# Kernel tuning notes

Hardware: AMD Instinct MI355X
Metric: run time of the kernel (lower is better)

Reference implementation:

```python
import jax, jax.numpy as jnp
import numpy as np

D_MODEL = 1024
N_HIDDEN = 64   # per-head dim (outer factor of packed proj dim)
N_HEAD = 16
B, L = 2, 2048


def setup_inputs() -> dict:
    key = jax.random.key(0)
    ks = jax.random.split(key, 7)
    s = 0.02
    return {
        "q": jax.random.normal(ks[0], (B, L, D_MODEL), dtype=jnp.float32),
        "k": jax.random.normal(ks[1], (B, L, D_MODEL), dtype=jnp.float32),
        "v": jax.random.normal(ks[2], (B, L, D_MODEL), dtype=jnp.float32),
        # torch nn.Linear weights: shape (out_features, in_features), y = x @ W.T
        "W_Q": jax.random.normal(ks[3], (N_HIDDEN * N_HEAD, D_MODEL), dtype=jnp.float32) * s,
        "W_K": jax.random.normal(ks[4], (N_HIDDEN * N_HEAD, D_MODEL), dtype=jnp.float32) * s,
        "W_V": jax.random.normal(ks[5], (N_HIDDEN * N_HEAD, D_MODEL), dtype=jnp.float32) * s,
        "W_O": jax.random.normal(ks[6], (D_MODEL, N_HEAD * N_HIDDEN), dtype=jnp.float32) * s,
    }


def reference(q, k, v, W_Q, W_K, W_V, W_O):
    b, l, _ = q.shape
    # projections (bias=False)
    qp = q @ W_Q.T  # [b,l,n_hidden*n_head]
    kp = k @ W_K.T
    vp = v @ W_V.T
    # rearrange 'b l (c h) -> b l c h' with c=n_hidden: hidden is OUTER factor
    qh = qp.reshape(b, l, N_HIDDEN, N_HEAD)
    kh = kp.reshape(b, l, N_HIDDEN, N_HEAD)
    vh = vp.reshape(b, l, N_HIDDEN, N_HEAD)
    scores = jnp.einsum('bldh,bjdh->bhlj', qh, kh) / np.float32(np.sqrt(N_HIDDEN))
    attn = jax.nn.softmax(scores, axis=-1)
    out = jnp.einsum('bhlj,bjdh->bldh', attn, vh)  # [b,l,n_hidden,n_head]
    out = out.reshape(b, l, N_HIDDEN * N_HEAD)      # 'b l d h -> b l (d h)'
    return out @ W_O.T
```

## Files before the change

### kernel.cpp

```cpp
#include <hip/hip_runtime.h>
#include <hip/hip_bf16.h>
#include <stdint.h>

typedef __attribute__((ext_vector_type(8))) short short8;
typedef __attribute__((ext_vector_type(4))) float f32x4;
typedef __attribute__((ext_vector_type(16))) float f32x16;
typedef __attribute__((ext_vector_type(2))) int int2v;
typedef unsigned short u16;
typedef unsigned int u32;


#define WAIT_VM8() do { asm volatile("s_waitcnt vmcnt(8)" ::: "memory"); \
                        __builtin_amdgcn_sched_barrier(0); } while (0)
#define WAIT_VM0() do { asm volatile("s_waitcnt vmcnt(0)" ::: "memory"); \
                        __builtin_amdgcn_sched_barrier(0); } while (0)
#define BARRIER()  do { __builtin_amdgcn_s_barrier(); \
                        __builtin_amdgcn_sched_barrier(0); } while (0)

__device__ __forceinline__ u16 bf16rne(float f) {
  u32 u = __builtin_bit_cast(u32, f);
  u += 0x7FFFu + ((u >> 16) & 1u);
  return (u16)(u >> 16);
}

__device__ __forceinline__ u32 cvtpk(float lo, float hi) {
  u32 r;
  asm("v_cvt_pk_bf16_f32 %0, %1, %2" : "=v"(r) : "v"(lo), "v"(hi));
  return r;
}

__device__ __forceinline__ void gl_lds16(const u16* g, u16* l) {
  __builtin_amdgcn_global_load_lds((const __attribute__((address_space(1))) void*)g,
                                   (__attribute__((address_space(3))) void*)l, 16, 0, 0);
}

struct CastArgs {
  const float* src[7];
  u16* dst[7];
  int n4[7];
};

__global__ void cast_all(CastArgs a) {
  const int id = blockIdx.y;
  const float* __restrict__ s = a.src[id];
  u16* __restrict__ d = a.dst[id];
  const int stride = gridDim.x * blockDim.x;
  const int i0 = blockIdx.x * blockDim.x + threadIdx.x;
  if (id < 6) {
    const int n4 = a.n4[id];
    for (int i = i0; i < n4; i += stride) {
      float4 v = ((const float4*)s)[i];
      u32 lo = (u32)bf16rne(v.x) | ((u32)bf16rne(v.y) << 16);
      u32 hi = (u32)bf16rne(v.z) | ((u32)bf16rne(v.w) << 16);
      ((uint2*)d)[i] = make_uint2(lo, hi);
    }
  } else {
    const int n = a.n4[6];
    for (int i = i0; i < n; i += stride) {
      int row = i >> 10, c = i & 1023;
      int hh = c >> 6, dd = c & 63;
      d[i] = bf16rne(s[(row << 10) + dd * 16 + hh]);
    }
  }
}

template<int AHEADS>
__device__ __forceinline__ void gemm_body(const u16* __restrict__ A, const u16* __restrict__ Bw,
                                          void* __restrict__ Cd, int epi, float ascale) {
  const int bn = blockIdx.x * 128, bm = blockIdx.y * 128;
  const int tid = threadIdx.x, lane = tid & 63, w = tid >> 6;
  const int wr = w >> 1, wc = w & 1;
  __shared__ __align__(16) u16 As[2][128 * 64];
  __shared__ __align__(16) u16 Bs[2][128 * 64];
  f32x4 acc[4][4];
#pragma unroll
  for (int m = 0; m < 4; ++m)
#pragma unroll
    for (int n = 0; n < 4; ++n) acc[m][n] = (f32x4){0.f, 0.f, 0.f, 0.f};

  auto STAGE = [&](int kt, int b) {
#pragma unroll
    for (int i = 0; i < 4; ++i) {
      int c = tid + i * 256;
      int row = c >> 3, kc = c & 7;
      int swz = (kc ^ (row & 7)) << 3;
      const u16* srcA;
      if (AHEADS) {
        int bA = bm >> 11;
        int lrow = (bm & 2047) + row;
        srcA = A + ((size_t)(bA * 16 + kt) * 2048 + lrow) * 64 + swz;
      } else {
        srcA = A + (size_t)(bm + row) * 1024 + kt * 64 + swz;
      }
      gl_lds16(srcA, &As[b][c * 8]);
      const u16* srcB = Bw + (size_t)(bn + row) * 1024 + kt * 64 + swz;
      gl_lds16(srcB, &Bs[b][c * 8]);
    }
  };

  auto COMPUTE = [&](int b) {
#pragma unroll
    for (int ks = 0; ks < 2; ++ks) {
      const int ck = ks * 4 + (lane >> 4);
      short8 af[4], bfr[4];
#pragma unroll
      for (int m = 0; m < 4; ++m) {
        int r = wr * 64 + m * 16 + (lane & 15);
        af[m] = *(const short8*)&As[b][(r * 8 + (ck ^ (r & 7))) * 8];
      }
#pragma unroll
      for (int n = 0; n < 4; ++n) {
        int r = wc * 64 + n * 16 + (lane & 15);
        bfr[n] = *(const short8*)&Bs[b][(r * 8 + (ck ^ (r & 7))) * 8];
      }
#pragma unroll
      for (int m = 0; m < 4; ++m)
#pragma unroll
        for (int n = 0; n < 4; ++n)
          acc[m][n] = __builtin_amdgcn_mfma_f32_16x16x32_bf16(af[m], bfr[n], acc[m][n], 0, 0, 0);
    }
  };

  STAGE(0, 0);
  STAGE(1, 1);
  for (int kt = 0; kt < 15; ++kt) {
    WAIT_VM8();
    BARRIER();
    COMPUTE(kt & 1);
    BARRIER();
    if (kt < 14) STAGE(kt + 2, kt & 1);
  }
  WAIT_VM0();
  BARRIER();
  COMPUTE(1);

  const int lrow4 = (lane >> 4) << 2;
  const int h = lane & 15;
  if (epi == 0) {
    u16* D = (u16*)Cd;
    const int dbase = (bn + wc * 64) >> 4;
#pragma unroll
    for (int m = 0; m < 4; ++m)
#pragma unroll
      for (int i = 0; i < 4; ++i) {
        int R = bm + wr * 64 + m * 16 + lrow4 + i;
        int b = R >> 11, l = R & 2047;
        u32 lo = (u32)bf16rne(acc[m][0][i] * ascale) | ((u32)bf16rne(acc[m][1][i] * ascale) << 16);
        u32 hi = (u32)bf16rne(acc[m][2][i] * ascale) | ((u32)bf16rne(acc[m][3][i] * ascale) << 16);
        size_t addr = ((size_t)((b * 16 + h) * 2048 + l)) * 64 + dbase;
        *(uint2*)(D + addr) = make_uint2(lo, hi);
      }
  } else if (epi == 1) {
    u16* D = (u16*)Cd;
    const int dbase = (bn + wc * 64) >> 4;
    const int b = bm >> 11;
#pragma unroll
    for (int m = 0; m < 4; ++m) {
      int l0 = (bm & 2047) + wr * 64 + m * 16 + lrow4;
#pragma unroll
      for (int n = 0; n < 4; ++n) {
        int d = dbase + n;
        u32 lo = (u32)bf16rne(acc[m][n][0]) | ((u32)bf16rne(acc[m][n][1]) << 16);
        u32 hi = (u32)bf16rne(acc[m][n][2]) | ((u32)bf16rne(acc[m][n][3]) << 16);
        size_t addr = ((size_t)((b * 16 + h) * 64 + d)) * 2048 + l0;
        *(uint2*)(D + addr) = make_uint2(lo, hi);
      }
    }
  } else {
    float* D = (float*)Cd;
#pragma unroll
    for (int m = 0; m < 4; ++m)
#pragma unroll
      for (int i = 0; i < 4; ++i) {
        int R = bm + wr * 64 + m * 16 + lrow4 + i;
        size_t base = (size_t)R * 1024 + bn + wc * 64 + (lane & 15);
#pragma unroll
        for (int n = 0; n < 4; ++n) D[base + n * 16] = acc[m][n][i];
      }
  }
}

struct ProjArgs { const u16* A[3]; const u16* W[3]; u16* D[3]; float scale[3]; };

__global__ __launch_bounds__(256, 2) void gemm_proj(ProjArgs pa) {
  const int z = blockIdx.z;
  gemm_body<0>(pa.A[z], pa.W[z], pa.D[z], z == 2 ? 1 : 0, pa.scale[z]);
}

__global__ __launch_bounds__(256, 2) void gemm_oproj(const u16* __restrict__ A,
                                                     const u16* __restrict__ W,
                                                     float* __restrict__ C) {
  gemm_body<1>(A, W, C, 2, 1.0f);
}

__global__ __launch_bounds__(128, 2) void attn_kernel(const u16* __restrict__ Qh,
                                                      const u16* __restrict__ Kh,
                                                      const u16* __restrict__ Vt,
                                                      u16* __restrict__ Oh) {
  const int hb = blockIdx.x;
  const int qt = blockIdx.y;
  const int tid = threadIdx.x, lane = tid & 63, w = tid >> 6;
  const int l31 = lane & 31, hi = lane >> 5;
  __shared__ __align__(16) u16 Ks[2][64 * 64];
  __shared__ __align__(16) u16 Vs[3][64 * 64];

  const u16* Qg = Qh + (size_t)hb * (2048 * 64);
  const u16* Kg = Kh + (size_t)hb * (2048 * 64);
  const u16* Vg = Vt + (size_t)hb * (64 * 2048);
  const int qrow = qt * 64 + w * 32 + l31;

  short8 qf[4];
#pragma unroll
  for (int ks = 0; ks < 4; ++ks)
    qf[ks] = *(const short8*)(Qg + (size_t)qrow * 64 + ks * 16 + hi * 8);

  int rs[4], sw[4];
#pragma unroll
  for (int i = 0; i < 4; ++i) {
    int c = tid + i * 128;
    rs[i] = c >> 3;
    sw[i] = (((c & 7) ^ (rs[i] & 7)) << 3);
  }

  auto STAGE_K = [&](int t, int slot) {
    const size_t ko = (size_t)t * (64 * 64);
#pragma unroll
    for (int i = 0; i < 4; ++i) {
      int c = tid + i * 128;
      gl_lds16(Kg + ko + (size_t)rs[i] * 64 + sw[i], &Ks[slot][c * 8]);
    }
  };
  auto STAGE_V = [&](int t, int slot) {
    const int vo = t * 64;
#pragma unroll
    for (int i = 0; i < 4; ++i) {
      int c = tid + i * 128;
      gl_lds16(Vg + (size_t)rs[i] * 2048 + vo + sw[i], &Vs[slot][c * 8]);
    }
  };

  f32x16 oacc0, oacc1, SA0, SA1, SB0, SB1;
#pragma unroll
  for (int i = 0; i < 16; ++i) { oacc0[i] = 0.f; oacc1[i] = 0.f; }
  u32 pkA[16], pkB[16];
  float lrow = 0.f;

  auto QKT = [&](int kslot, f32x16& s0, f32x16& s1) {
#pragma unroll
    for (int i = 0; i < 16; ++i) { s0[i] = 0.f; s1[i] = 0.f; }
    __builtin_amdgcn_s_setprio(1);
#pragma unroll
    for (int ks = 0; ks < 4; ++ks) {
      const int ck = 2 * ks + hi;
      const int r0 = l31, r1 = 32 + l31;
      short8 k0 = *(const short8*)&Ks[kslot][(r0 * 8 + (ck ^ (r0 & 7))) * 8];
      short8 k1 = *(const short8*)&Ks[kslot][(r1 * 8 + (ck ^ (r1 & 7))) * 8];
      s0 = __builtin_amdgcn_mfma_f32_32x32x16_bf16(k0, qf[ks], s0, 0, 0, 0);
      s1 = __builtin_amdgcn_mfma_f32_32x32x16_bf16(k1, qf[ks], s1, 0, 0, 0);
    }
    __builtin_amdgcn_s_setprio(0);
  };

  auto PV = [&](const u32* pk, int vslot) {
    __builtin_amdgcn_s_setprio(1);
#pragma unroll
    for (int c = 0; c < 4; ++c) {
      union { u32 wu[4]; short8 v; } un;
      un.wu[0] = pk[c * 4 + 0]; un.wu[1] = pk[c * 4 + 1];
      un.wu[2] = pk[c * 4 + 2]; un.wu[3] = pk[c * 4 + 3];
      const int ckv = 2 * c + hi;
      const int rv0 = l31, rv1 = 32 + l31;
      short8 v0 = *(const short8*)&Vs[vslot][(rv0 * 8 + (ckv ^ (rv0 & 7))) * 8];
      short8 v1 = *(const short8*)&Vs[vslot][(rv1 * 8 + (ckv ^ (rv1 & 7))) * 8];
      oacc0 = __builtin_amdgcn_mfma_f32_32x32x16_bf16(v0, un.v, oacc0, 0, 0, 0);
      oacc1 = __builtin_amdgcn_mfma_f32_32x32x16_bf16(v1, un.v, oacc1, 0, 0, 0);
    }
    __builtin_amdgcn_s_setprio(0);
  };

  auto SOFTMAX = [&](f32x16& s0, f32x16& s1, u32* pk) {
#pragma unroll
    for (int i = 0; i < 16; ++i) {
      s0[i] = __builtin_amdgcn_exp2f(s0[i]);
      s1[i] = __builtin_amdgcn_exp2f(s1[i]);
    }
    f32x16 a01 = s0 + s1;
    float r8[8];
#pragma unroll
    for (int i = 0; i < 8; ++i) r8[i] = a01[i] + a01[i + 8];
#pragma unroll
    for (int i = 0; i < 4; ++i) r8[i] += r8[i + 4];
    float rsum = (r8[0] + r8[1]) + (r8[2] + r8[3]);
    int2v pr = __builtin_amdgcn_permlane32_swap(__builtin_bit_cast(int, rsum),
                                                __builtin_bit_cast(int, rsum), false, false);
    lrow += __builtin_bit_cast(float, pr[0]) + __builtin_bit_cast(float, pr[1]);
#pragma unroll
    for (int c = 0; c < 4; ++c) {
      float pe0, pe1, pe2, pe3, pe4, pe5, pe6, pe7;
      if (c < 2) {
        const int s8 = (c & 1) * 8;
        pe0 = s0[s8 + 0]; pe1 = s0[s8 + 1]; pe2 = s0[s8 + 2]; pe3 = s0[s8 + 3];
        pe4 = s0[s8 + 4]; pe5 = s0[s8 + 5]; pe6 = s0[s8 + 6]; pe7 = s0[s8 + 7];
      } else {
        const int s8 = (c & 1) * 8;
        pe0 = s1[s8 + 0]; pe1 = s1[s8 + 1]; pe2 = s1[s8 + 2]; pe3 = s1[s8 + 3];
        pe4 = s1[s8 + 4]; pe5 = s1[s8 + 5]; pe6 = s1[s8 + 6]; pe7 = s1[s8 + 7];
      }
      u32 a0 = cvtpk(pe0, pe1), a1 = cvtpk(pe2, pe3);
      u32 a2 = cvtpk(pe4, pe5), a3 = cvtpk(pe6, pe7);
      int2v w02 = __builtin_amdgcn_permlane32_swap((int)a0, (int)a2, false, false);
      int2v w13 = __builtin_amdgcn_permlane32_swap((int)a1, (int)a3, false, false);
      pk[c * 4 + 0] = (u32)w02[0]; pk[c * 4 + 1] = (u32)w13[0];
      pk[c * 4 + 2] = (u32)w02[1]; pk[c * 4 + 3] = (u32)w13[1];
    }
  };

  STAGE_K(0, 0); STAGE_K(1, 1); STAGE_V(0, 0);
  WAIT_VM8(); BARRIER();
  QKT(0, SA0, SA1);
  BARRIER();
  STAGE_K(2, 0); STAGE_V(1, 1);
  WAIT_VM8(); BARRIER();
  QKT(1, SB0, SB1);
  SOFTMAX(SA0, SA1, pkB);
  BARRIER();
  STAGE_K(3, 1); STAGE_V(2, 2);

  for (int i = 2; i < 32; i += 2) {
    WAIT_VM8(); BARRIER();
    QKT(0, SA0, SA1);
    PV(pkB, (i - 2) % 3);
    SOFTMAX(SB0, SB1, pkA);
    BARRIER();
    if (i + 2 <= 31) STAGE_K(i + 2, 0);
    STAGE_V(i + 1, (i + 1) % 3);
    WAIT_VM8(); BARRIER();
    QKT(1, SB0, SB1);
    PV(pkA, (i - 1) % 3);
    SOFTMAX(SA0, SA1, pkB);
    BARRIER();
    if (i + 3 <= 31) STAGE_K(i + 3, 1);
    if (i + 2 <= 31) STAGE_V(i + 2, (i + 2) % 3);
  }

  WAIT_VM0(); BARRIER();
  SOFTMAX(SB0, SB1, pkA);
  PV(pkB, 30 % 3);
  PV(pkA, 31 % 3);

  const float inv = 1.0f / lrow;
  u16* Og = Oh + (size_t)hb * (2048 * 64) + (size_t)qrow * 64;
#pragma unroll
  for (int dblk = 0; dblk < 2; ++dblk) {
#pragma unroll
    for (int r = 0; r < 16; r += 2) {
      const int d = dblk * 32 + (r & 3) + 8 * (r >> 2) + 4 * hi;
      float v0 = (dblk ? oacc1[r] : oacc0[r]) * inv;
      float v1 = (dblk ? oacc1[r + 1] : oacc0[r + 1]) * inv;
      *(u32*)(Og + d) = (u32)bf16rne(v0) | ((u32)bf16rne(v1) << 16);
    }
  }
}

extern "C" void kernel_launch(void* const* d_in, const int* in_sizes, int n_in,
                              void* d_out, int out_size, void* d_ws, size_t ws_size,
                              hipStream_t stream) {
  const float* q = (const float*)d_in[0];
  const float* k = (const float*)d_in[1];
  const float* v = (const float*)d_in[2];
  const float* WQ = (const float*)d_in[3];
  const float* WK = (const float*)d_in[4];
  const float* WV = (const float*)d_in[5];
  const float* WO = (const float*)d_in[6];
  float* out = (float*)d_out;
  char* ws = (char*)d_ws;
  const size_t MB = 1024 * 1024;
  if (ws_size < 64 * MB) return;

  u16* qb  = (u16*)(ws + 0 * MB);
  u16* kb  = (u16*)(ws + 8 * MB);
  u16* vb  = (u16*)(ws + 16 * MB);
  u16* WQb = (u16*)(ws + 24 * MB);
  u16* WKb = (u16*)(ws + 26 * MB);
  u16* WVb = (u16*)(ws + 28 * MB);
  u16* WOt = (u16*)(ws + 30 * MB);
  u16* Qh  = (u16*)(ws + 32 * MB);
  u16* Kh  = (u16*)(ws + 40 * MB);
  u16* Vt  = (u16*)(ws + 48 * MB);
  u16* Ohd = (u16*)(ws + 56 * MB);

  CastArgs ca;
  ca.src[0] = q;  ca.dst[0] = qb;  ca.n4[0] = (4096 * 1024) / 4;
  ca.src[1] = k;  ca.dst[1] = kb;  ca.n4[1] = (4096 * 1024) / 4;
  ca.src[2] = v;  ca.dst[2] = vb;  ca.n4[2] = (4096 * 1024) / 4;
  ca.src[3] = WQ; ca.dst[3] = WQb; ca.n4[3] = (1024 * 1024) / 4;
  ca.src[4] = WK; ca.dst[4] = WKb; ca.n4[4] = (1024 * 1024) / 4;
  ca.src[5] = WV; ca.dst[5] = WVb; ca.n4[5] = (1024 * 1024) / 4;
  ca.src[6] = WO; ca.dst[6] = WOt; ca.n4[6] = 1024 * 1024;
  cast_all<<<dim3(256, 7), 256, 0, stream>>>(ca);

  ProjArgs pa;
  pa.A[0] = qb; pa.W[0] = WQb; pa.D[0] = Qh;  pa.scale[0] = 0.18033688011f;
  pa.A[1] = kb; pa.W[1] = WKb; pa.D[1] = Kh;  pa.scale[1] = 1.0f;
  pa.A[2] = vb; pa.W[2] = WVb; pa.D[2] = Vt;  pa.scale[2] = 1.0f;
  gemm_proj<<<dim3(8, 32, 3), 256, 0, stream>>>(pa);

  attn_kernel<<<dim3(32, 32), 128, 0, stream>>>(Qh, Kh, Vt, Ohd);

  gemm_oproj<<<dim3(8, 32), 256, 0, stream>>>(Ohd, WOt, out);
}
```

Measured before the change: 135.3 us.

## Fuse fp32-to-bf16 activation cast into projection GEMM A-tile loading

```diff
diff --git a/kernel.cpp b/kernel.cpp
--- a/kernel.cpp
+++ b/kernel.cpp
@@ -10,12 +10,17 @@
 typedef unsigned int u32;
 
 
-#define WAIT_VM8() do { asm volatile("s_waitcnt vmcnt(8)" ::: "memory"); \
-                        __builtin_amdgcn_sched_barrier(0); } while (0)
-#define WAIT_VM0() do { asm volatile("s_waitcnt vmcnt(0)" ::: "memory"); \
-                        __builtin_amdgcn_sched_barrier(0); } while (0)
-#define BARRIER()  do { __builtin_amdgcn_s_barrier(); \
-                        __builtin_amdgcn_sched_barrier(0); } while (0)
+#define WAIT_VM12() do { asm volatile("s_waitcnt vmcnt(12)" ::: "memory"); \
+                         __builtin_amdgcn_sched_barrier(0); } while (0)
+#define WAIT_VM8()  do { asm volatile("s_waitcnt vmcnt(8)" ::: "memory"); \
+                         __builtin_amdgcn_sched_barrier(0); } while (0)
+#define WAIT_VM0()  do { asm volatile("s_waitcnt vmcnt(0)" ::: "memory"); \
+                         __builtin_amdgcn_sched_barrier(0); } while (0)
+#define BARRIER()   do { __builtin_amdgcn_s_barrier(); \
+                         __builtin_amdgcn_sched_barrier(0); } while (0)
+#define LGKM0_BAR() do { asm volatile("s_waitcnt lgkmcnt(0)" ::: "memory"); \
+                         __builtin_amdgcn_s_barrier(); \
+                         __builtin_amdgcn_sched_barrier(0); } while (0)
 
 __device__ __forceinline__ u16 bf16rne(float f) {
   u32 u = __builtin_bit_cast(u32, f);
@@ -35,9 +40,9 @@
 }
 
 struct CastArgs {
-  const float* src[7];
-  u16* dst[7];
-  int n4[7];
+  const float* src[4];
+  u16* dst[4];
+  int n4[4];
 };
 
 __global__ void cast_all(CastArgs a) {
@@ -46,7 +51,7 @@
   u16* __restrict__ d = a.dst[id];
   const int stride = gridDim.x * blockDim.x;
   const int i0 = blockIdx.x * blockDim.x + threadIdx.x;
-  if (id < 6) {
+  if (id < 3) {
     const int n4 = a.n4[id];
     for (int i = i0; i < n4; i += stride) {
       float4 v = ((const float4*)s)[i];
@@ -55,7 +60,7 @@
       ((uint2*)d)[i] = make_uint2(lo, hi);
     }
   } else {
-    const int n = a.n4[6];
+    const int n = a.n4[3];
     for (int i = i0; i < n; i += stride) {
       int row = i >> 10, c = i & 1023;
       int hh = c >> 6, dd = c & 63;
@@ -64,9 +69,144 @@
   }
 }
 
-template<int AHEADS>
-__device__ __forceinline__ void gemm_body(const u16* __restrict__ A, const u16* __restrict__ Bw,
-                                          void* __restrict__ Cd, int epi, float ascale) {
+struct ProjFArgs { const float* A[3]; const u16* W[3]; u16* D[3]; float scale[3]; };
+
+__global__ __launch_bounds__(256, 2) void gemm_projf(ProjFArgs pa) {
+  const int bid = blockIdx.x;
+  const int grp = ((bid >> 6) << 3) | (bid & 7);
+  const int bn = ((bid >> 3) & 7) * 128;
+  const int z = grp >> 5;
+  const int bm = (grp & 31) * 128;
+  const float* __restrict__ A = pa.A[z];
+  const u16* __restrict__ Bw = pa.W[z];
+  u16* __restrict__ D = pa.D[z];
+  const float ascale = pa.scale[z];
+  const int epi = (z == 2) ? 1 : 0;
+
+  const int tid = threadIdx.x, lane = tid & 63, w = tid >> 6;
+  const int wr = w >> 1, wc = w & 1;
+  __shared__ __align__(16) u16 As[2][128 * 64];
+  __shared__ __align__(16) u16 Bs[2][128 * 64];
+
+  f32x4 acc[4][4];
+#pragma unroll
+  for (int m = 0; m < 4; ++m)
+#pragma unroll
+    for (int n = 0; n < 4; ++n) acc[m][n] = (f32x4){0.f, 0.f, 0.f, 0.f};
+
+  struct ARegs { float4 v[8]; };
+  ARegs RA, RB;
+
+  auto STAGE_A = [&](int kt, ARegs& R) {
+#pragma unroll
+    for (int i = 0; i < 4; ++i) {
+      int c = tid + i * 256;
+      int row = c >> 3;
+      int col = (((c & 7) ^ (row & 7)) << 3);
+      const float* src = A + (size_t)(bm + row) * 1024 + kt * 64 + col;
+      R.v[2 * i] = *(const float4*)(src);
+      R.v[2 * i + 1] = *(const float4*)(src + 4);
+    }
+  };
+  auto WRITE_A = [&](ARegs& R, int b) {
+#pragma unroll
+    for (int i = 0; i < 4; ++i) {
+      int c = tid + i * 256;
+      u32 p0 = (u32)bf16rne(R.v[2 * i].x) | ((u32)bf16rne(R.v[2 * i].y) << 16);
+      u32 p1 = (u32)bf16rne(R.v[2 * i].z) | ((u32)bf16rne(R.v[2 * i].w) << 16);
+      u32 p2 = (u32)bf16rne(R.v[2 * i + 1].x) | ((u32)bf16rne(R.v[2 * i + 1].y) << 16);
+      u32 p3 = (u32)bf16rne(R.v[2 * i + 1].z) | ((u32)bf16rne(R.v[2 * i + 1].w) << 16);
+      *(uint4*)&As[b][c * 8] = make_uint4(p0, p1, p2, p3);
+    }
+  };
+  auto STAGE_B = [&](int kt, int b) {
+#pragma unroll
+    for (int i = 0; i < 4; ++i) {
+      int c = tid + i * 256;
+      int row = c >> 3;
+      int swz = (((c & 7) ^ (row & 7)) << 3);
+      gl_lds16(Bw + (size_t)(bn + row) * 1024 + kt * 64 + swz, &Bs[b][c * 8]);
+    }
+  };
+  auto COMPUTE = [&](int b) {
+#pragma unroll
+    for (int ks = 0; ks < 2; ++ks) {
+      const int ck = ks * 4 + (lane >> 4);
+      short8 af[4], bfr[4];
+#pragma unroll
+      for (int m = 0; m < 4; ++m) {
+        int r = wr * 64 + m * 16 + (lane & 15);
+        af[m] = *(const short8*)&As[b][(r * 8 + (ck ^ (r & 7))) * 8];
+      }
+#pragma unroll
+      for (int n = 0; n < 4; ++n) {
+        int r = wc * 64 + n * 16 + (lane & 15);
+        bfr[n] = *(const short8*)&Bs[b][(r * 8 + (ck ^ (r & 7))) * 8];
+      }
+#pragma unroll
+      for (int m = 0; m < 4; ++m)
+#pragma unroll
+        for (int n = 0; n < 4; ++n)
+          acc[m][n] = __builtin_amdgcn_mfma_f32_16x16x32_bf16(af[m], bfr[n], acc[m][n], 0, 0, 0);
+    }
+  };
+
+  STAGE_A(0, RA); STAGE_B(0, 0);
+  STAGE_A(1, RB); STAGE_B(1, 1);
+  for (int k2 = 0; k2 < 7; ++k2) {
+    const int kt = 2 * k2;
+    WAIT_VM12();
+    WRITE_A(RA, 0); LGKM0_BAR();
+    COMPUTE(0); BARRIER();
+    STAGE_A(kt + 2, RA); STAGE_B(kt + 2, 0);
+    WAIT_VM12();
+    WRITE_A(RB, 1); LGKM0_BAR();
+    COMPUTE(1); BARRIER();
+    STAGE_A(kt + 3, RB); STAGE_B(kt + 3, 1);
+  }
+  WAIT_VM12();
+  WRITE_A(RA, 0); LGKM0_BAR();
+  COMPUTE(0); BARRIER();
+  WAIT_VM0();
+  WRITE_A(RB, 1); LGKM0_BAR();
+  COMPUTE(1);
+
+  const int lrow4 = (lane >> 4) << 2;
+  const int h = lane & 15;
+  if (epi == 0) {
+    const int dbase = (bn + wc * 64) >> 4;
+#pragma unroll
+    for (int m = 0; m < 4; ++m)
+#pragma unroll
+      for (int i = 0; i < 4; ++i) {
+        int R = bm + wr * 64 + m * 16 + lrow4 + i;
+        int b = R >> 11, l = R & 2047;
+        u32 lo = (u32)bf16rne(acc[m][0][i] * ascale) | ((u32)bf16rne(acc[m][1][i] * ascale) << 16);
+        u32 hi = (u32)bf16rne(acc[m][2][i] * ascale) | ((u32)bf16rne(acc[m][3][i] * ascale) << 16);
+        size_t addr = ((size_t)((b * 16 + h) * 2048 + l)) * 64 + dbase;
+        *(uint2*)(D + addr) = make_uint2(lo, hi);
+      }
+  } else {
+    const int dbase = (bn + wc * 64) >> 4;
+    const int b = bm >> 11;
+#pragma unroll
+    for (int m = 0; m < 4; ++m) {
+      int l0 = (bm & 2047) + wr * 64 + m * 16 + lrow4;
+#pragma unroll
+      for (int n = 0; n < 4; ++n) {
+        int d = dbase + n;
+        u32 lo = (u32)bf16rne(acc[m][n][0]) | ((u32)bf16rne(acc[m][n][1]) << 16);
+        u32 hi = (u32)bf16rne(acc[m][n][2]) | ((u32)bf16rne(acc[m][n][3]) << 16);
+        size_t addr = ((size_t)((b * 16 + h) * 64 + d)) * 2048 + l0;
+        *(uint2*)(D + addr) = make_uint2(lo, hi);
+      }
+    }
+  }
+}
+
+__global__ __launch_bounds__(256, 2) void gemm_oproj(const u16* __restrict__ A,
+                                                     const u16* __restrict__ Bw,
+                                                     float* __restrict__ C) {
   const int bn = blockIdx.x * 128, bm = blockIdx.y * 128;
   const int tid = threadIdx.x, lane = tid & 63, w = tid >> 6;
   const int wr = w >> 1, wc = w & 1;
@@ -84,14 +224,9 @@
       int c = tid + i * 256;
       int row = c >> 3, kc = c & 7;
       int swz = (kc ^ (row & 7)) << 3;
-      const u16* srcA;
-      if (AHEADS) {
-        int bA = bm >> 11;
-        int lrow = (bm & 2047) + row;
-        srcA = A + ((size_t)(bA * 16 + kt) * 2048 + lrow) * 64 + swz;
-      } else {
-        srcA = A + (size_t)(bm + row) * 1024 + kt * 64 + swz;
-      }
+      int bA = bm >> 11;
+      int lrow = (bm & 2047) + row;
+      const u16* srcA = A + ((size_t)(bA * 16 + kt) * 2048 + lrow) * 64 + swz;
       gl_lds16(srcA, &As[b][c * 8]);
       const u16* srcB = Bw + (size_t)(bn + row) * 1024 + kt * 64 + swz;
       gl_lds16(srcB, &Bs[b][c * 8]);
@@ -135,62 +270,15 @@
   COMPUTE(1);
 
   const int lrow4 = (lane >> 4) << 2;
-  const int h = lane & 15;
-  if (epi == 0) {
-    u16* D = (u16*)Cd;
-    const int dbase = (bn + wc * 64) >> 4;
-#pragma unroll
-    for (int m = 0; m < 4; ++m)
-#pragma unroll
-      for (int i = 0; i < 4; ++i) {
-        int R = bm + wr * 64 + m * 16 + lrow4 + i;
-        int b = R >> 11, l = R & 2047;
-        u32 lo = (u32)bf16rne(acc[m][0][i] * ascale) | ((u32)bf16rne(acc[m][1][i] * ascale) << 16);
-        u32 hi = (u32)bf16rne(acc[m][2][i] * ascale) | ((u32)bf16rne(acc[m][3][i] * ascale) << 16);
-        size_t addr = ((size_t)((b * 16 + h) * 2048 + l)) * 64 + dbase;
-        *(uint2*)(D + addr) = make_uint2(lo, hi);
-      }
-  } else if (epi == 1) {
-    u16* D = (u16*)Cd;
-    const int dbase = (bn + wc * 64) >> 4;
-    const int b = bm >> 11;
-#pragma unroll
-    for (int m = 0; m < 4; ++m) {
-      int l0 = (bm & 2047) + wr * 64 + m * 16 + lrow4;
-#pragma unroll
-      for (int n = 0; n < 4; ++n) {
-        int d = dbase + n;
-        u32 lo = (u32)bf16rne(acc[m][n][0]) | ((u32)bf16rne(acc[m][n][1]) << 16);
-        u32 hi = (u32)bf16rne(acc[m][n][2]) | ((u32)bf16rne(acc[m][n][3]) << 16);
-        size_t addr = ((size_t)((b * 16 + h) * 64 + d)) * 2048 + l0;
-        *(uint2*)(D + addr) = make_uint2(lo, hi);
-      }
-    }
-  } else {
-    float* D = (float*)Cd;
-#pragma unroll
-    for (int m = 0; m < 4; ++m)
-#pragma unroll
-      for (int i = 0; i < 4; ++i) {
-        int R = bm + wr * 64 + m * 16 + lrow4 + i;
-        size_t base = (size_t)R * 1024 + bn + wc * 64 + (lane & 15);
-#pragma unroll
-        for (int n = 0; n < 4; ++n) D[base + n * 16] = acc[m][n][i];
-      }
-  }
-}
-
-struct ProjArgs { const u16* A[3]; const u16* W[3]; u16* D[3]; float scale[3]; };
-
-__global__ __launch_bounds__(256, 2) void gemm_proj(ProjArgs pa) {
-  const int z = blockIdx.z;
-  gemm_body<0>(pa.A[z], pa.W[z], pa.D[z], z == 2 ? 1 : 0, pa.scale[z]);
-}
-
-__global__ __launch_bounds__(256, 2) void gemm_oproj(const u16* __restrict__ A,
-                                                     const u16* __restrict__ W,
-                                                     float* __restrict__ C) {
-  gemm_body<1>(A, W, C, 2, 1.0f);
+#pragma unroll
+  for (int m = 0; m < 4; ++m)
+#pragma unroll
+    for (int i = 0; i < 4; ++i) {
+      int R = bm + wr * 64 + m * 16 + lrow4 + i;
+      size_t base = (size_t)R * 1024 + bn + wc * 64 + (lane & 15);
+#pragma unroll
+      for (int n = 0; n < 4; ++n) C[base + n * 16] = acc[m][n][i];
+    }
 }
 
 __global__ __launch_bounds__(128, 2) void attn_kernel(const u16* __restrict__ Qh,
@@ -377,9 +465,6 @@
   const size_t MB = 1024 * 1024;
   if (ws_size < 64 * MB) return;
 
-  u16* qb  = (u16*)(ws + 0 * MB);
-  u16* kb  = (u16*)(ws + 8 * MB);
-  u16* vb  = (u16*)(ws + 16 * MB);
   u16* WQb = (u16*)(ws + 24 * MB);
   u16* WKb = (u16*)(ws + 26 * MB);
   u16* WVb = (u16*)(ws + 28 * MB);
@@ -390,20 +475,17 @@
   u16* Ohd = (u16*)(ws + 56 * MB);
 
   CastArgs ca;
-  ca.src[0] = q;  ca.dst[0] = qb;  ca.n4[0] = (4096 * 1024) / 4;
-  ca.src[1] = k;  ca.dst[1] = kb;  ca.n4[1] = (4096 * 1024) / 4;
-  ca.src[2] = v;  ca.dst[2] = vb;  ca.n4[2] = (4096 * 1024) / 4;
-  ca.src[3] = WQ; ca.dst[3] = WQb; ca.n4[3] = (1024 * 1024) / 4;
-  ca.src[4] = WK; ca.dst[4] = WKb; ca.n4[4] = (1024 * 1024) / 4;
-  ca.src[5] = WV; ca.dst[5] = WVb; ca.n4[5] = (1024 * 1024) / 4;
-  ca.src[6] = WO; ca.dst[6] = WOt; ca.n4[6] = 1024 * 1024;
-  cast_all<<<dim3(256, 7), 256, 0, stream>>>(ca);
-
-  ProjArgs pa;
-  pa.A[0] = qb; pa.W[0] = WQb; pa.D[0] = Qh;  pa.scale[0] = 0.18033688011f;
-  pa.A[1] = kb; pa.W[1] = WKb; pa.D[1] = Kh;  pa.scale[1] = 1.0f;
-  pa.A[2] = vb; pa.W[2] = WVb; pa.D[2] = Vt;  pa.scale[2] = 1.0f;
-  gemm_proj<<<dim3(8, 32, 3), 256, 0, stream>>>(pa);
+  ca.src[0] = WQ; ca.dst[0] = WQb; ca.n4[0] = (1024 * 1024) / 4;
+  ca.src[1] = WK; ca.dst[1] = WKb; ca.n4[1] = (1024 * 1024) / 4;
+  ca.src[2] = WV; ca.dst[2] = WVb; ca.n4[2] = (1024 * 1024) / 4;
+  ca.src[3] = WO; ca.dst[3] = WOt; ca.n4[3] = 1024 * 1024;
+  cast_all<<<dim3(128, 4), 256, 0, stream>>>(ca);
+
+  ProjFArgs pa;
+  pa.A[0] = q; pa.W[0] = WQb; pa.D[0] = Qh;  pa.scale[0] = 0.18033688011f;
+  pa.A[1] = k; pa.W[1] = WKb; pa.D[1] = Kh;  pa.scale[1] = 1.0f;
+  pa.A[2] = v; pa.W[2] = WVb; pa.D[2] = Vt;  pa.scale[2] = 1.0f;
+  gemm_projf<<<768, 256, 0, stream>>>(pa);
 
   attn_kernel<<<dim3(32, 32), 128, 0, stream>>>(Qh, Kh, Vt, Ohd);
 
```

New measurement: 131.1 us. 3.1% less time.
